# Optimization experiments

Measured on AMD Instinct MI355X. Metric: run time of the kernel, lower is better.

Reference implementation:

```python
import jax, jax.numpy as jnp
import numpy as np

TEMPERATURE = 0.07
EPS = 1e-8  # torch F.cosine_similarity eps


def _normalize(x):
    # x: [B, D] -> row-normalized with torch-style eps clamp on the norm
    n = jnp.sqrt(jnp.sum(x * x, axis=-1, keepdims=True))
    return x / jnp.maximum(n, EPS)


def setup_inputs() -> dict:
    key = jax.random.key(0)
    k1, k2, k3 = jax.random.split(key, 3)
    B, D, C = 8192, 512, 2048
    return {
        "label_tensor": jax.random.randint(k1, (B,), 0, C, dtype=jnp.int64),
        "feature_a": jax.random.normal(k2, (B, D), dtype=jnp.float32),
        "feature_b": jax.random.normal(k3, (B, D), dtype=jnp.float32),
    }


def reference(label_tensor, feature_a, feature_b):
    # cosine similarity matrix: cos_score[i, j] = cos(a_i, b_j)  -> [B, B]
    a = _normalize(feature_a)
    b = _normalize(feature_b)
    cos_score = jnp.einsum('id,jd->ij', a, b)

    logits = cos_score / TEMPERATURE
    # positives mask: same label (diagonal always True since label[i]==label[i])
    mask = (label_tensor[:, None] == label_tensor[None, :])

    e = jnp.exp(logits)                      # safe: |logits| <= 1/0.07 ~ 14.3
    numerator = jnp.sum(jnp.where(mask, e, 0.0), axis=1)
    denominator = jnp.sum(e, axis=1)
    loss = -jnp.mean(jnp.log(numerator / denominator))
    return loss, cos_score
```

## Files before the change

kernel.cpp:

```cpp
#include <hip/hip_runtime.h>
#include <cstdint>
#include <cstddef>

#define BDIM 8192
#define DDIM 512

typedef __bf16 bf16x8 __attribute__((ext_vector_type(8)));
typedef float f32x4 __attribute__((ext_vector_type(4)));

__device__ inline unsigned short f32_to_bf16(float f) {
    unsigned int u = __float_as_uint(f);
    u += 0x7FFF + ((u >> 16) & 1);
    return (unsigned short)(u >> 16);
}

__global__ __launch_bounds__(256) void normalize_kernel(
    const float* __restrict__ a, const float* __restrict__ b,
    unsigned short* __restrict__ an, unsigned short* __restrict__ bn)
{
    const int lane = threadIdx.x & 63;
    const int row = blockIdx.x * 4 + (threadIdx.x >> 6);
    const float* src;
    unsigned short* dst;
    if (row < BDIM) {
        src = a + (size_t)row * DDIM;
        dst = an + (size_t)row * DDIM;
    } else {
        src = b + (size_t)(row - BDIM) * DDIM;
        dst = bn + (size_t)(row - BDIM) * DDIM;
    }
    const float4* s4 = (const float4*)src;
    float4 v0 = s4[lane];
    float4 v1 = s4[lane + 64];
    float ss = v0.x * v0.x + v0.y * v0.y + v0.z * v0.z + v0.w * v0.w
             + v1.x * v1.x + v1.y * v1.y + v1.z * v1.z + v1.w * v1.w;
#pragma unroll
    for (int m = 1; m < 64; m <<= 1) ss += __shfl_xor(ss, m);
    float inv = 1.0f / fmaxf(sqrtf(ss), 1e-8f);
    ushort4 o0, o1;
    o0.x = f32_to_bf16(v0.x * inv); o0.y = f32_to_bf16(v0.y * inv);
    o0.z = f32_to_bf16(v0.z * inv); o0.w = f32_to_bf16(v0.w * inv);
    o1.x = f32_to_bf16(v1.x * inv); o1.y = f32_to_bf16(v1.y * inv);
    o1.z = f32_to_bf16(v1.z * inv); o1.w = f32_to_bf16(v1.w * inv);
    ushort4* d4 = (ushort4*)dst;
    d4[lane] = o0;
    d4[lane + 64] = o1;
}

#define BAR()    __builtin_amdgcn_s_barrier()
#define WAITV4() asm volatile("s_waitcnt vmcnt(4)" ::: "memory")
#define WAITV0() asm volatile("s_waitcnt vmcnt(0)" ::: "memory")

__global__ __launch_bounds__(512, 2) void gemm_fused_kernel(
    const unsigned short* __restrict__ an, const unsigned short* __restrict__ bn,
    const int* __restrict__ labels, float* __restrict__ cos_out,
    float* __restrict__ num, float* __restrict__ den)
{
    __shared__ __align__(16) char lds[131072];
    char* ldsC = (char*)lds;

    const int t = threadIdx.x;
    const int wid = t >> 6;
    const int lane = t & 63;
    const int quad = lane >> 4;
    const int lr = lane & 15;
    const int sx = lr & 7;
    const int bm = blockIdx.y;
    const int bnb = blockIdx.x;
    const int wm = wid >> 2;
    const int wn = wid & 3;

    f32x4 acc[8][4] = {};

    unsigned rowOff[2], ldsW[2];
#pragma unroll
    for (int j = 0; j < 2; ++j) {
        int li = (j * 8 + wid) * 64 + lane;
        int r  = li >> 3;
        int gc = (li & 7) ^ (r & 7);
        rowOff[j] = (unsigned)(r * (DDIM * 2) + gc * 16);
        ldsW[j]   = (unsigned)((j * 8 + wid) * 1024);
    }
    const char* aT = (const char*)an + (size_t)(bm * 256) * (DDIM * 2);
    const char* bT = (const char*)bn + (size_t)(bnb * 256) * (DDIM * 2);

    auto STG = [&](int i) {
        const int tile = i >> 2, role = i & 3;
        const int isA = (role == 1 || role == 2);
        const int h   = (role == 2 || role == 3);
        const unsigned ldsBase = (unsigned)((tile & 1) * 65536) +
                                 (isA ? 0u : 32768u) + (unsigned)(h * 16384);
        const char* g = (isA ? aT : bT) + h * (128 * DDIM * 2) + tile * 128;
        __builtin_amdgcn_global_load_lds(
            (const __attribute__((address_space(1))) void*)(g + rowOff[0]),
            (__attribute__((address_space(3))) void*)(ldsC + ldsBase + ldsW[0]), 16, 0, 0);
        __builtin_amdgcn_global_load_lds(
            (const __attribute__((address_space(1))) void*)(g + rowOff[1]),
            (__attribute__((address_space(3))) void*)(ldsC + ldsBase + ldsW[1]), 16, 0, 0);
    };

    bf16x8 afA[4][2], afB[4][2], bfA[2][2], bfB[2][2];

    auto MMAQ = [&](int mh, int nh, bf16x8 (&afX)[4][2], bf16x8 (&bfX)[2][2]) {
        __builtin_amdgcn_s_setprio(1);
#pragma unroll
        for (int kk = 0; kk < 2; ++kk)
#pragma unroll
            for (int mi = 0; mi < 4; ++mi)
#pragma unroll
                for (int ni = 0; ni < 2; ++ni)
                    acc[mh * 4 + mi][nh * 2 + ni] =
                        __builtin_amdgcn_mfma_f32_16x16x32_bf16(
                            afX[mi][kk], bfX[ni][kk],
                            acc[mh * 4 + mi][nh * 2 + ni], 0, 0, 0);
        __builtin_amdgcn_s_setprio(0);
    };

    STG(0); STG(1); STG(2); STG(3); STG(4); STG(5);
    WAITV4();
    BAR();

#pragma unroll
    for (int T = 0; T < 8; ++T) {
        const unsigned bufO  = (unsigned)((T & 1) * 65536);
        const unsigned aBase = bufO + (unsigned)(wm * 16384);
        const unsigned bBase = bufO + 32768u + (unsigned)((wn >> 1) * 16384);
        const int brp = (wn & 1) * 64;

#pragma unroll
        for (int mi = 0; mi < 4; ++mi)
#pragma unroll
            for (int kk = 0; kk < 2; ++kk) {
                int rp = mi * 16 + lr;
                afA[mi][kk] = *(const bf16x8*)(ldsC + aBase + rp * 128 +
                                               (((kk * 4 + quad) ^ sx) << 4));
            }
#pragma unroll
        for (int ni = 0; ni < 2; ++ni)
#pragma unroll
            for (int kk = 0; kk < 2; ++kk) {
                int rp = brp + ni * 16 + lr;
                bfA[ni][kk] = *(const bf16x8*)(ldsC + bBase + rp * 128 +
                                               (((kk * 4 + quad) ^ sx) << 4));
            }
        if (6 + 4 * T < 32) STG(6 + 4 * T);
        BAR();
        MMAQ(0, 0, afA, bfA);
        BAR();

#pragma unroll
        for (int ni = 0; ni < 2; ++ni)
#pragma unroll
            for (int kk = 0; kk < 2; ++kk) {
                int rp = brp + (ni + 2) * 16 + lr;
                bfB[ni][kk] = *(const bf16x8*)(ldsC + bBase + rp * 128 +
                                               (((kk * 4 + quad) ^ sx) << 4));
            }
        if (7 + 4 * T < 32) STG(7 + 4 * T);
        BAR();
        MMAQ(0, 1, afA, bfB);
        BAR();

#pragma unroll
        for (int mi = 0; mi < 4; ++mi)
#pragma unroll
            for (int kk = 0; kk < 2; ++kk) {
                int rp = (mi + 4) * 16 + lr;
                afB[mi][kk] = *(const bf16x8*)(ldsC + aBase + rp * 128 +
                                               (((kk * 4 + quad) ^ sx) << 4));
            }
        if (8 + 4 * T < 32) STG(8 + 4 * T);
        BAR();
        MMAQ(1, 1, afB, bfB);
        BAR();

        if (9 + 4 * T < 32) STG(9 + 4 * T);
        BAR();
        MMAQ(1, 0, afB, bfA);
        if (T < 6) { WAITV4(); BAR(); }
        else if (T == 6) { WAITV0(); BAR(); }
    }

    const float INV_T = 1.0f / 0.07f;
    const int col0 = bnb * 256 + wn * 64 + lr;
    int lab_c[4];
#pragma unroll
    for (int ni = 0; ni < 4; ++ni) lab_c[ni] = labels[col0 + ni * 16];

#pragma unroll
    for (int mi = 0; mi < 8; ++mi) {
        int rbase = bm * 256 + wm * 128 + mi * 16 + quad * 4;
#pragma unroll
        for (int r = 0; r < 4; ++r) {
            int row = rbase + r;
            int lab_r = labels[row];
            float dsum = 0.0f, nsum = 0.0f;
#pragma unroll
            for (int ni = 0; ni < 4; ++ni) {
                float cv = acc[mi][ni][r];
                __builtin_nontemporal_store(cv, &cos_out[(size_t)row * BDIM + col0 + ni * 16]);
                float e = __expf(cv * INV_T);
                dsum += e;
                nsum += (lab_c[ni] == lab_r) ? e : 0.0f;
            }
#pragma unroll
            for (int m = 1; m < 16; m <<= 1) {
                dsum += __shfl_xor(dsum, m);
                nsum += __shfl_xor(nsum, m);
            }
            if (lr == 0) {
                atomicAdd(&den[row], dsum);
                atomicAdd(&num[row], nsum);
            }
        }
    }
}

__global__ __launch_bounds__(1024) void loss_kernel(
    const float* __restrict__ num, const float* __restrict__ den,
    float* __restrict__ out)
{
    int t = threadIdx.x;
    float s = 0.0f;
#pragma unroll
    for (int i = 0; i < 8; ++i) {
        int idx = t + i * 1024;
        s += __logf(num[idx] / den[idx]);
    }
#pragma unroll
    for (int m = 1; m < 64; m <<= 1) s += __shfl_xor(s, m);
    __shared__ float red[16];
    if ((t & 63) == 0) red[t >> 6] = s;
    __syncthreads();
    if (t == 0) {
        float tot = 0.0f;
#pragma unroll
        for (int i = 0; i < 16; ++i) tot += red[i];
        out[0] = -tot / (float)BDIM;
    }
}

extern "C" void kernel_launch(void* const* d_in, const int* in_sizes, int n_in,
                              void* d_out, int out_size, void* d_ws, size_t ws_size,
                              hipStream_t stream)
{
    const int* labels = (const int*)d_in[0];
    const float* fa = (const float*)d_in[1];
    const float* fb = (const float*)d_in[2];
    float* out = (float*)d_out;

    unsigned short* an = (unsigned short*)d_ws;
    unsigned short* bn = an + (size_t)BDIM * DDIM;
    float* num = (float*)(bn + (size_t)BDIM * DDIM);
    float* den = num + BDIM;

    hipMemsetAsync(num, 0, 2 * BDIM * sizeof(float), stream);
    normalize_kernel<<<4096, 256, 0, stream>>>(fa, fb, an, bn);
    dim3 grid(32, 32);
    gemm_fused_kernel<<<grid, 512, 0, stream>>>(an, bn, labels, out + 1, num, den);
    loss_kernel<<<1, 1024, 0, stream>>>(num, den, out);
}
```

Before: 417.5 us.

## Stage cos tile through LDS for vector stores and reduce atomics per block

```diff
diff --git a/kernel.cpp b/kernel.cpp
--- a/kernel.cpp
+++ b/kernel.cpp
@@ -187,19 +187,25 @@
 #pragma unroll
     for (int ni = 0; ni < 4; ++ni) lab_c[ni] = labels[col0 + ni * 16];
 
+    float* patch = (float*)(ldsC + wid * 4096);
+    float* part  = (float*)(ldsC + 32768);
+
 #pragma unroll
     for (int mi = 0; mi < 8; ++mi) {
-        int rbase = bm * 256 + wm * 128 + mi * 16 + quad * 4;
+#pragma unroll
+        for (int ni = 0; ni < 4; ++ni)
+#pragma unroll
+            for (int r = 0; r < 4; ++r)
+                patch[(quad * 4 + r) * 64 + ni * 16 + lr] = acc[mi][ni][r];
+
 #pragma unroll
         for (int r = 0; r < 4; ++r) {
-            int row = rbase + r;
-            int lab_r = labels[row];
+            int rowL = wm * 128 + mi * 16 + quad * 4 + r;
+            int lab_r = labels[bm * 256 + rowL];
             float dsum = 0.0f, nsum = 0.0f;
 #pragma unroll
             for (int ni = 0; ni < 4; ++ni) {
-                float cv = acc[mi][ni][r];
-                __builtin_nontemporal_store(cv, &cos_out[(size_t)row * BDIM + col0 + ni * 16]);
-                float e = __expf(cv * INV_T);
+                float e = __expf(acc[mi][ni][r] * INV_T);
                 dsum += e;
                 nsum += (lab_c[ni] == lab_r) ? e : 0.0f;
             }
@@ -209,10 +215,29 @@
                 nsum += __shfl_xor(nsum, m);
             }
             if (lr == 0) {
-                atomicAdd(&den[row], dsum);
-                atomicAdd(&num[row], nsum);
+                float2 pv; pv.x = nsum; pv.y = dsum;
+                *(float2*)&part[(size_t)(wn * 256 + rowL) * 2] = pv;
             }
         }
+
+#pragma unroll
+        for (int p = 0; p < 4; ++p) {
+            f32x4 v = *(const f32x4*)&patch[(p * 4 + quad) * 64 + lr * 4];
+            int row = bm * 256 + wm * 128 + mi * 16 + p * 4 + quad;
+            f32x4* gp = (f32x4*)&cos_out[(size_t)row * BDIM + bnb * 256 + wn * 64 + lr * 4];
+            __builtin_nontemporal_store(v, gp);
+        }
+    }
+
+    __syncthreads();
+    if (t < 256) {
+        float2 p0 = *(float2*)&part[(size_t)(0 * 256 + t) * 2];
+        float2 p1 = *(float2*)&part[(size_t)(1 * 256 + t) * 2];
+        float2 p2 = *(float2*)&part[(size_t)(2 * 256 + t) * 2];
+        float2 p3 = *(float2*)&part[(size_t)(3 * 256 + t) * 2];
+        int row = bm * 256 + t;
+        atomicAdd(&num[row], p0.x + p1.x + p2.x + p3.x);
+        atomicAdd(&den[row], p0.y + p1.y + p2.y + p3.y);
     }
 }
 
```

New measurement: 390.9 us. 6.4% less time.
